# Kernel tuning notes

Hardware: AMD Instinct MI355X
Metric: run time of the kernel (lower is better)

## Reference

```python
import jax, jax.numpy as jnp
import numpy as np

B, S, D, H = 2, 2048, 1024, 16
DH = D // H  # per-head depth = 64


def setup_inputs() -> dict:
    key = jax.random.key(0)
    ks = jax.random.split(key, 10)
    s = 1.0 / np.sqrt(D)
    return {
        "q_in": jax.random.normal(ks[0], (B, S, D), jnp.float32),
        "k_in": jax.random.normal(ks[1], (B, S, D), jnp.float32),
        "v_in": jax.random.normal(ks[2], (B, S, D), jnp.float32),
        "mask": jnp.zeros((B, 1, S, S), jnp.float32),
        "Wq": jax.random.normal(ks[3], (D, D), jnp.float32) * s,
        "bq": jnp.zeros((D,), jnp.float32),
        "Wk": jax.random.normal(ks[4], (D, D), jnp.float32) * s,
        "bk": jnp.zeros((D,), jnp.float32),
        "Wv": jax.random.normal(ks[5], (D, D), jnp.float32) * s,
        "bv": jnp.zeros((D,), jnp.float32),
        "Wo": jax.random.normal(ks[6], (D, D), jnp.float32) * s,
        "bo": jnp.zeros((D,), jnp.float32),
    }


def _split_heads(x):
    # [B,S,D] -> [B,H,S,DH]
    b, s, _ = x.shape
    return x.reshape(b, s, H, DH).transpose(0, 2, 1, 3)


def reference(q_in, k_in, v_in, mask, Wq, bq, Wk, bk, Wv, bv, Wo, bo):
    q = _split_heads(q_in @ Wq + bq)
    k = _split_heads(k_in @ Wk + bk)
    v = _split_heads(v_in @ Wv + bv)
    logits = jnp.einsum("bhqd,bhkd->bhqk", q, k) / jnp.sqrt(jnp.float32(DH))
    logits = logits + mask * -1e9
    attn = jax.nn.softmax(logits, axis=-1)
    ctx = jnp.einsum("bhqk,bhkd->bhqd", attn, v)  # [B,H,S,DH]
    concat = ctx.transpose(0, 2, 1, 3).reshape(q_in.shape[0], -1, D)
    out = concat @ Wo + bo  # dropout is identity at inference
    return out, attn
```

## Files before the change

kernel.cpp:

```cpp
#include <hip/hip_runtime.h>
#include <hip/hip_bf16.h>

static constexpr int cB = 2, cS = 2048, cD = 1024, cH = 16, cDH = 64;

typedef __attribute__((ext_vector_type(4))) float f32x4;
typedef __attribute__((ext_vector_type(8))) short s16x8;
typedef unsigned long long u64;
typedef unsigned short u16;

__device__ inline f32x4 mfma16(s16x8 a, s16x8 b, f32x4 c) {
  return __builtin_amdgcn_mfma_f32_16x16x32_bf16(a, b, c, 0, 0, 0);
}

__device__ inline u16 f2bf(float x) {
  unsigned u = __float_as_uint(x);
  u += 0x7FFFu + ((u >> 16) & 1u);
  return (u16)(u >> 16);
}

__device__ inline unsigned cvt_pk_bf16(float lo, float hi) {
  unsigned r;
  asm("v_cvt_pk_bf16_f32 %0, %1, %2" : "=v"(r) : "v"(lo), "v"(hi));
  return r;
}

__device__ inline f32x4 zero4() { f32x4 z; z[0] = z[1] = z[2] = z[3] = 0.f; return z; }

__device__ inline void gload16(const void* src, void* dst) {
  __builtin_amdgcn_global_load_lds((const __attribute__((address_space(1))) void*)src,
                                   (__attribute__((address_space(3))) void*)dst, 16, 0, 0);
}

__global__ __launch_bounds__(256) void wt4_kernel(const float* __restrict__ W0,
                                                  const float* __restrict__ W1,
                                                  const float* __restrict__ W2,
                                                  const float* __restrict__ W3,
                                                  u16* __restrict__ T0, u16* __restrict__ T1,
                                                  u16* __restrict__ T2, u16* __restrict__ T3) {
  __shared__ float tile[32][33];
  int z = blockIdx.z;
  const float* W = z == 0 ? W0 : z == 1 ? W1 : z == 2 ? W2 : W3;
  u16* Wt = z == 0 ? T0 : z == 1 ? T1 : z == 2 ? T2 : T3;
  int tx = threadIdx.x, ty = threadIdx.y;
  int r0 = blockIdx.y * 32, c0 = blockIdx.x * 32;
  for (int i = ty; i < 32; i += 8)
    tile[i][tx] = W[(size_t)(r0 + i) * cD + c0 + tx];
  __syncthreads();
  for (int i = ty; i < 32; i += 8)
    Wt[(size_t)(c0 + i) * cD + r0 + tx] = f2bf(tile[tx][i]);
}

__global__ __launch_bounds__(256) void maskflag_kernel(const float* __restrict__ mask,
                                                       unsigned char* __restrict__ flags) {
  int blk = blockIdx.x;
  int b = blk >> 10, qt = (blk >> 5) & 31, kt = blk & 31;
  int t = threadIdx.x;
  int r = t >> 2, c0 = (t & 3) * 16;
  const float4* p = (const float4*)(mask + ((size_t)b * cS + qt * 64 + r) * cS + kt * 64 + c0);
  int any = 0;
  for (int j = 0; j < 4; ++j) {
    float4 v = p[j];
    any |= (v.x != 0.f) | (v.y != 0.f) | (v.z != 0.f) | (v.w != 0.f);
  }
  __shared__ int sred;
  if (t == 0) sred = 0;
  __syncthreads();
  if (any) atomicOr(&sred, 1);
  __syncthreads();
  if (t == 0) flags[blk] = (unsigned char)sred;
}

template<bool AFP32, bool OUTF32, int BN>
__device__ __forceinline__ void gemm_body(const void* __restrict__ Ap,
                                          const u16* __restrict__ Bt,
                                          const float* __restrict__ bias,
                                          void* __restrict__ outp,
                                          float scale, int vt_mode, int bidx,
                                          u16* As, u16* Bs) {
  constexpr int NI = BN / 32;
  constexpr int RPW = BN / 4;
  int t = threadIdx.x;
  int w = t >> 6, l = t & 63, g = l >> 4, li = l & 15;
  int bm = bidx & 31, bn = bidx >> 5;
  int m0 = bm * 128, n0 = bn * BN;
  int wr = w >> 1, wc = w & 1;

  f32x4 acc[4][NI];
  for (int i = 0; i < 4; ++i)
    for (int j = 0; j < NI; ++j) acc[i][j] = zero4();

  for (int kk = 0; kk < cD; kk += 64) {
    if (AFP32) {
      const float* X = (const float*)Ap;
      int ar = t >> 1, ak0 = (t & 1) * 32;
      const float* asrc = X + (size_t)(m0 + ar) * cD + kk + ak0;
      int sw = ar & 7;
      for (int j = 0; j < 4; ++j) {
        float4 x0 = ((const float4*)asrc)[2 * j];
        float4 x1 = ((const float4*)asrc)[2 * j + 1];
        union { s16x8 v; unsigned u[4]; } s;
        s.u[0] = cvt_pk_bf16(x0.x, x0.y);
        s.u[1] = cvt_pk_bf16(x0.z, x0.w);
        s.u[2] = cvt_pk_bf16(x1.x, x1.y);
        s.u[3] = cvt_pk_bf16(x1.z, x1.w);
        int chunk = (ak0 >> 3) + j;
        *(s16x8*)&As[ar * 64 + ((chunk ^ sw) * 8)] = s.v;
      }
    } else {
      const u16* X = (const u16*)Ap;
      for (int is = 0; is < 4; ++is) {
        int row = w * 32 + is * 8 + (l >> 3);
        int chunk = l & 7;
        const u16* src = X + (size_t)(m0 + row) * cD + kk + ((chunk ^ (row & 7)) * 8);
        gload16(src, &As[(w * 32 + is * 8) * 64]);
      }
    }
    for (int is = 0; is < RPW / 8; ++is) {
      int row = w * RPW + is * 8 + (l >> 3);
      int chunk = l & 7;
      const u16* src = Bt + (size_t)(n0 + row) * cD + kk + ((chunk ^ (row & 7)) * 8);
      gload16(src, &Bs[(w * RPW + is * 8) * 64]);
    }
    __syncthreads();
    for (int c = 0; c < 2; ++c) {
      s16x8 af[4], bf[NI];
      for (int mi = 0; mi < 4; ++mi) {
        int r = wr * 64 + mi * 16 + li;
        af[mi] = *(const s16x8*)&As[r * 64 + (((c * 4 + g) ^ (r & 7)) * 8)];
      }
      for (int ni = 0; ni < NI; ++ni) {
        int r = wc * (BN / 2) + ni * 16 + li;
        bf[ni] = *(const s16x8*)&Bs[r * 64 + (((c * 4 + g) ^ (r & 7)) * 8)];
      }
      for (int mi = 0; mi < 4; ++mi)
        for (int ni = 0; ni < NI; ++ni)
          acc[mi][ni] = mfma16(af[mi], bf[ni], acc[mi][ni]);
    }
    __syncthreads();
  }

  for (int ni = 0; ni < NI; ++ni) {
    int n = n0 + wc * (BN / 2) + ni * 16 + li;
    float bv = bias[n];
    for (int mi = 0; mi < 4; ++mi) {
      for (int r = 0; r < 4; ++r) {
        int m = m0 + wr * 64 + mi * 16 + g * 4 + r;
        float val = acc[mi][ni][r] + bv;
        if (OUTF32) {
          ((float*)outp)[(size_t)m * cD + n] = val;
        } else {
          val *= scale;
          int b = m >> 11, s = m & 2047;
          int h = n >> 6, d = n & 63;
          size_t idx = vt_mode ? ((size_t)(b * cH + h) * cDH + d) * cS + s
                               : ((size_t)(b * cH + h) * cS + s) * cDH + d;
          ((u16*)outp)[idx] = f2bf(val);
        }
      }
    }
  }
}

__global__ __launch_bounds__(256) void qkv_gemm(const float* __restrict__ Xq,
                                                const float* __restrict__ Xk,
                                                const float* __restrict__ Xv,
                                                const u16* __restrict__ Btq,
                                                const u16* __restrict__ Btk,
                                                const u16* __restrict__ Btv,
                                                const float* __restrict__ bq,
                                                const float* __restrict__ bk,
                                                const float* __restrict__ bv,
                                                u16* __restrict__ oq,
                                                u16* __restrict__ ok,
                                                u16* __restrict__ ov) {
  __shared__ __attribute__((aligned(16))) u16 As[128 * 64];
  __shared__ __attribute__((aligned(16))) u16 Bs[128 * 64];
  int which = blockIdx.x >> 8, bidx = blockIdx.x & 255;
  const float* X = which == 0 ? Xq : which == 1 ? Xk : Xv;
  const u16* Bt = which == 0 ? Btq : which == 1 ? Btk : Btv;
  const float* bias = which == 0 ? bq : which == 1 ? bk : bv;
  u16* o = which == 0 ? oq : which == 1 ? ok : ov;
  float scale = which == 0 ? 0.125f : 1.0f;
  int vt = which == 2 ? 1 : 0;
  gemm_body<true, false, 128>(X, Bt, bias, o, scale, vt, bidx, As, Bs);
}

__global__ __launch_bounds__(256) void out_gemm(const u16* __restrict__ Xc,
                                                const u16* __restrict__ Bt,
                                                const float* __restrict__ bias,
                                                float* __restrict__ outp) {
  __shared__ __attribute__((aligned(16))) u16 As[128 * 64];
  __shared__ __attribute__((aligned(16))) u16 Bs[64 * 64];
  gemm_body<false, true, 64>(Xc, Bt, bias, outp, 1.0f, 0, blockIdx.x, As, Bs);
}

__global__ __launch_bounds__(512) void attn_kernel(const u16* __restrict__ Q,
                                                   const u16* __restrict__ K,
                                                   const u16* __restrict__ Vt,
                                                   const float* __restrict__ mask,
                                                   const unsigned char* __restrict__ flags,
                                                   float* __restrict__ attn,
                                                   u16* __restrict__ ctx) {
  __shared__ __attribute__((aligned(16))) u16 Kl[2][64 * 64];
  __shared__ __attribute__((aligned(16))) u16 Vl[2][64 * 64];
  int t = threadIdx.x;
  int w = t >> 6, l = t & 63, g = l >> 4, li = l & 15;
  int p = blockIdx.x;
  int blk = (p & 7) * 64 + (p >> 3);
  int bh = blk >> 4, qt = blk & 15;
  int b = bh >> 4;
  int qbase = qt * 128;
  const u16* Qh = Q + (size_t)bh * cS * cDH;
  const u16* Kh = K + (size_t)bh * cS * cDH;
  const u16* Vh = Vt + (size_t)bh * cDH * cS;
  const unsigned char* fl = flags + (b << 10) + ((qbase + w * 16) >> 6) * 32;

  s16x8 qf[2];
  {
    const u16* qp = Qh + (size_t)(qbase + w * 16 + li) * cDH;
    qf[0] = *(const s16x8*)(qp + 8 * g);
    qf[1] = *(const s16x8*)(qp + 32 + 8 * g);
  }
  int srow8 = l >> 3, schunk = l & 7;
  int q_lane = qbase + w * 16 + li;
  int srow = w * 8 + srow8;
  const u16* kstage = Kh + (size_t)srow * cDH + ((schunk ^ (srow & 7)) * 8);
  const u16* vstage = Vh + (size_t)srow * cS + ((schunk ^ (srow & 7)) * 8);
  u16* kl_dst = &Kl[0][(w * 8) * 64];
  u16* vl_dst = &Vl[0][(w * 8) * 64];
  const int KSTEP = 64 * cDH;

  gload16(kstage, kl_dst);
  asm volatile("s_waitcnt vmcnt(0)" ::: "memory");
  __builtin_amdgcn_sched_barrier(0);
  __builtin_amdgcn_s_barrier();
  __builtin_amdgcn_sched_barrier(0);
  float racc4[4] = {0.f, 0.f, 0.f, 0.f};
  for (int kt = 0; kt < 32; ++kt) {
    int cur = kt & 1;
    if (kt + 1 < 32)
      gload16(kstage + (size_t)(kt + 1) * KSTEP, kl_dst + (cur ^ 1) * 64 * 64);
    f32x4 acc[4];
    for (int mt = 0; mt < 4; ++mt) acc[mt] = zero4();
    for (int c = 0; c < 2; ++c)
      for (int mt = 0; mt < 4; ++mt) {
        int r = mt * 16 + li;
        s16x8 kf = *(const s16x8*)&Kl[cur][r * 64 + (((c * 4 + g) ^ (r & 7)) * 8)];
        acc[mt] = mfma16(kf, qf[c], acc[mt]);
      }
    bool um = fl[kt] != 0;
    for (int mt = 0; mt < 4; ++mt)
      for (int r = 0; r < 4; ++r) {
        float lv = acc[mt][r];
        if (um) lv += mask[((size_t)b * cS + q_lane) * cS + kt * 64 + mt * 16 + 4 * g + r] * -1e9f;
        racc4[r] += __expf(lv);
      }
    if (kt + 1 < 32) {
      asm volatile("s_waitcnt vmcnt(0)" ::: "memory");
      __builtin_amdgcn_sched_barrier(0);
      __builtin_amdgcn_s_barrier();
      __builtin_amdgcn_sched_barrier(0);
    }
  }
  float racc = (racc4[0] + racc4[1]) + (racc4[2] + racc4[3]);
  racc += __shfl_xor(racc, 16, 64);
  racc += __shfl_xor(racc, 32, 64);
  float lr = __logf(racc);

  f32x4 cacc[4];
  for (int dt = 0; dt < 4; ++dt) cacc[dt] = zero4();
  float* attn_row = attn + (size_t)bh * cS * cS + (size_t)q_lane * cS;
  gload16(kstage, kl_dst);
  gload16(vstage, vl_dst);
  asm volatile("s_waitcnt vmcnt(0)" ::: "memory");
  __builtin_amdgcn_sched_barrier(0);
  __builtin_amdgcn_s_barrier();
  __builtin_amdgcn_sched_barrier(0);
  for (int kt = 0; kt < 32; ++kt) {
    int cur = kt & 1;
    if (kt + 1 < 32) {
      gload16(kstage + (size_t)(kt + 1) * KSTEP, kl_dst + (cur ^ 1) * 64 * 64);
      gload16(vstage + (kt + 1) * 64, vl_dst + (cur ^ 1) * 64 * 64);
    }
    f32x4 acc[4];
    for (int mt = 0; mt < 4; ++mt) acc[mt] = zero4();
    for (int c = 0; c < 2; ++c)
      for (int mt = 0; mt < 4; ++mt) {
        int r = mt * 16 + li;
        s16x8 kf = *(const s16x8*)&Kl[cur][r * 64 + (((c * 4 + g) ^ (r & 7)) * 8)];
        acc[mt] = mfma16(kf, qf[c], acc[mt]);
      }
    bool um = fl[kt] != 0;
    s16x8 pa[2];
    for (int c = 0; c < 2; ++c) {
      union { s16x8 v; unsigned u[4]; } pk;
      f32x4 pvq[2];
      for (int hh = 0; hh < 2; ++hh) {
        int mt = c * 2 + hh;
        for (int r = 0; r < 4; ++r) {
          float lv = acc[mt][r];
          if (um) lv += mask[((size_t)b * cS + q_lane) * cS + kt * 64 + mt * 16 + 4 * g + r] * -1e9f;
          pvq[hh][r] = __expf(lv - lr);
        }
        __builtin_nontemporal_store(pvq[hh], (f32x4*)(attn_row + kt * 64 + mt * 16 + 4 * g));
      }
      pk.u[0] = cvt_pk_bf16(pvq[0][0], pvq[0][1]);
      pk.u[1] = cvt_pk_bf16(pvq[0][2], pvq[0][3]);
      pk.u[2] = cvt_pk_bf16(pvq[1][0], pvq[1][1]);
      pk.u[3] = cvt_pk_bf16(pvq[1][2], pvq[1][3]);
      pa[c] = pk.v;
    }
    for (int c = 0; c < 2; ++c) {
      for (int dt = 0; dt < 4; ++dt) {
        int row = dt * 16 + li;
        const u16* rb = &Vl[cur][row * 64];
        int o0 = (((c * 4 + 0 + (g >> 1)) ^ (li & 7)) * 8) + (g & 1) * 4;
        int o1 = (((c * 4 + 2 + (g >> 1)) ^ (li & 7)) * 8) + (g & 1) * 4;
        union { s16x8 v; u64 qq[2]; } vf;
        vf.qq[0] = *(const u64*)(rb + o0);
        vf.qq[1] = *(const u64*)(rb + o1);
        cacc[dt] = mfma16(pa[c], vf.v, cacc[dt]);
      }
    }
    if (kt + 1 < 32) {
      asm volatile("s_waitcnt vmcnt(4)" ::: "memory");
      __builtin_amdgcn_sched_barrier(0);
      __builtin_amdgcn_s_barrier();
      __builtin_amdgcn_sched_barrier(0);
    }
  }

  int h = bh & 15;
  for (int dt = 0; dt < 4; ++dt)
    for (int r = 0; r < 4; ++r) {
      int s = qbase + w * 16 + g * 4 + r;
      int d = dt * 16 + li;
      ctx[((size_t)(b * cS + s)) * cD + h * 64 + d] = f2bf(cacc[dt][r]);
    }
}

extern "C" void kernel_launch(void* const* d_in, const int* in_sizes, int n_in,
                              void* d_out, int out_size, void* d_ws, size_t ws_size,
                              hipStream_t stream) {
  const float* q_in = (const float*)d_in[0];
  const float* k_in = (const float*)d_in[1];
  const float* v_in = (const float*)d_in[2];
  const float* mask = (const float*)d_in[3];
  const float* Wq = (const float*)d_in[4];
  const float* bq = (const float*)d_in[5];
  const float* Wk = (const float*)d_in[6];
  const float* bk = (const float*)d_in[7];
  const float* Wv = (const float*)d_in[8];
  const float* bv = (const float*)d_in[9];
  const float* Wo = (const float*)d_in[10];
  const float* bo = (const float*)d_in[11];

  float* out = (float*)d_out;
  float* attn = out + (size_t)cB * cS * cD;

  const size_t MATB = (size_t)cB * cS * cD * 2;
  const size_t WB = (size_t)cD * cD * 2;
  char* ws = (char*)d_ws;
  u16* WqT = (u16*)(ws);
  u16* WkT = (u16*)(ws + WB);
  u16* WvT = (u16*)(ws + 2 * WB);
  u16* WoT = (u16*)(ws + 3 * WB);
  u16* wsQ  = (u16*)(ws + 4 * WB);
  u16* wsK  = (u16*)(ws + 4 * WB + MATB);
  u16* wsVt = (u16*)(ws + 4 * WB + 2 * MATB);
  u16* wsC  = (u16*)(ws + 4 * WB + 3 * MATB);
  unsigned char* flags = (unsigned char*)(ws + 4 * WB + 4 * MATB);
  const size_t REQUIRED = 4 * WB + 4 * MATB + 2048;
  if (ws_size < REQUIRED) return;

  dim3 tb(32, 8);
  wt4_kernel<<<dim3(32, 32, 4), tb, 0, stream>>>(Wq, Wk, Wv, Wo, WqT, WkT, WvT, WoT);
  maskflag_kernel<<<2048, 256, 0, stream>>>(mask, flags);

  qkv_gemm<<<768, 256, 0, stream>>>(q_in, k_in, v_in, WqT, WkT, WvT,
                                    bq, bk, bv, wsQ, wsK, wsVt);

  attn_kernel<<<512, 512, 0, stream>>>(wsQ, wsK, wsVt, mask, flags, attn, wsC);

  out_gemm<<<512, 256, 0, stream>>>(wsC, WoT, bo, out);
}
```

Baseline: 336.4 us.

## Pre-convert QKV inputs to bf16 and load via direct global-to-LDS copies

```diff
diff --git a/kernel.cpp b/kernel.cpp
--- a/kernel.cpp
+++ b/kernel.cpp
@@ -29,6 +29,26 @@
 __device__ inline void gload16(const void* src, void* dst) {
   __builtin_amdgcn_global_load_lds((const __attribute__((address_space(1))) void*)src,
                                    (__attribute__((address_space(3))) void*)dst, 16, 0, 0);
+}
+
+__global__ __launch_bounds__(256) void xcvt_kernel(const float* __restrict__ X0,
+                                                   const float* __restrict__ X1,
+                                                   const float* __restrict__ X2,
+                                                   u16* __restrict__ Y0,
+                                                   u16* __restrict__ Y1,
+                                                   u16* __restrict__ Y2) {
+  int z = blockIdx.z;
+  const float* X = z == 0 ? X0 : z == 1 ? X1 : X2;
+  u16* Y = z == 0 ? Y0 : z == 1 ? Y1 : Y2;
+  size_t i = ((size_t)blockIdx.x * 256 + threadIdx.x) * 8;
+  float4 a = *(const float4*)(X + i);
+  float4 b = *(const float4*)(X + i + 4);
+  union { s16x8 v; unsigned u[4]; } s;
+  s.u[0] = cvt_pk_bf16(a.x, a.y);
+  s.u[1] = cvt_pk_bf16(a.z, a.w);
+  s.u[2] = cvt_pk_bf16(b.x, b.y);
+  s.u[3] = cvt_pk_bf16(b.z, b.w);
+  *(s16x8*)(Y + i) = s.v;
 }
 
 __global__ __launch_bounds__(256) void wt4_kernel(const float* __restrict__ W0,
@@ -70,8 +90,8 @@
   if (t == 0) flags[blk] = (unsigned char)sred;
 }
 
-template<bool AFP32, bool OUTF32, int BN>
-__device__ __forceinline__ void gemm_body(const void* __restrict__ Ap,
+template<bool OUTF32, int BN>
+__device__ __forceinline__ void gemm_body(const u16* __restrict__ X,
                                           const u16* __restrict__ Bt,
                                           const float* __restrict__ bias,
                                           void* __restrict__ outp,
@@ -90,30 +110,11 @@
     for (int j = 0; j < NI; ++j) acc[i][j] = zero4();
 
   for (int kk = 0; kk < cD; kk += 64) {
-    if (AFP32) {
-      const float* X = (const float*)Ap;
-      int ar = t >> 1, ak0 = (t & 1) * 32;
-      const float* asrc = X + (size_t)(m0 + ar) * cD + kk + ak0;
-      int sw = ar & 7;
-      for (int j = 0; j < 4; ++j) {
-        float4 x0 = ((const float4*)asrc)[2 * j];
-        float4 x1 = ((const float4*)asrc)[2 * j + 1];
-        union { s16x8 v; unsigned u[4]; } s;
-        s.u[0] = cvt_pk_bf16(x0.x, x0.y);
-        s.u[1] = cvt_pk_bf16(x0.z, x0.w);
-        s.u[2] = cvt_pk_bf16(x1.x, x1.y);
-        s.u[3] = cvt_pk_bf16(x1.z, x1.w);
-        int chunk = (ak0 >> 3) + j;
-        *(s16x8*)&As[ar * 64 + ((chunk ^ sw) * 8)] = s.v;
-      }
-    } else {
-      const u16* X = (const u16*)Ap;
-      for (int is = 0; is < 4; ++is) {
-        int row = w * 32 + is * 8 + (l >> 3);
-        int chunk = l & 7;
-        const u16* src = X + (size_t)(m0 + row) * cD + kk + ((chunk ^ (row & 7)) * 8);
-        gload16(src, &As[(w * 32 + is * 8) * 64]);
-      }
+    for (int is = 0; is < 4; ++is) {
+      int row = w * 32 + is * 8 + (l >> 3);
+      int chunk = l & 7;
+      const u16* src = X + (size_t)(m0 + row) * cD + kk + ((chunk ^ (row & 7)) * 8);
+      gload16(src, &As[(w * 32 + is * 8) * 64]);
     }
     for (int is = 0; is < RPW / 8; ++is) {
       int row = w * RPW + is * 8 + (l >> 3);
@@ -161,9 +162,9 @@
   }
 }
 
-__global__ __launch_bounds__(256) void qkv_gemm(const float* __restrict__ Xq,
-                                                const float* __restrict__ Xk,
-                                                const float* __restrict__ Xv,
+__global__ __launch_bounds__(256) void qkv_gemm(const u16* __restrict__ Xq,
+                                                const u16* __restrict__ Xk,
+                                                const u16* __restrict__ Xv,
                                                 const u16* __restrict__ Btq,
                                                 const u16* __restrict__ Btk,
                                                 const u16* __restrict__ Btv,
@@ -176,13 +177,13 @@
   __shared__ __attribute__((aligned(16))) u16 As[128 * 64];
   __shared__ __attribute__((aligned(16))) u16 Bs[128 * 64];
   int which = blockIdx.x >> 8, bidx = blockIdx.x & 255;
-  const float* X = which == 0 ? Xq : which == 1 ? Xk : Xv;
+  const u16* X = which == 0 ? Xq : which == 1 ? Xk : Xv;
   const u16* Bt = which == 0 ? Btq : which == 1 ? Btk : Btv;
   const float* bias = which == 0 ? bq : which == 1 ? bk : bv;
   u16* o = which == 0 ? oq : which == 1 ? ok : ov;
   float scale = which == 0 ? 0.125f : 1.0f;
   int vt = which == 2 ? 1 : 0;
-  gemm_body<true, false, 128>(X, Bt, bias, o, scale, vt, bidx, As, Bs);
+  gemm_body<false, 128>(X, Bt, bias, o, scale, vt, bidx, As, Bs);
 }
 
 __global__ __launch_bounds__(256) void out_gemm(const u16* __restrict__ Xc,
@@ -191,7 +192,7 @@
                                                 float* __restrict__ outp) {
   __shared__ __attribute__((aligned(16))) u16 As[128 * 64];
   __shared__ __attribute__((aligned(16))) u16 Bs[64 * 64];
-  gemm_body<false, true, 64>(Xc, Bt, bias, outp, 1.0f, 0, blockIdx.x, As, Bs);
+  gemm_body<true, 64>(Xc, Bt, bias, outp, 1.0f, 0, blockIdx.x, As, Bs);
 }
 
 __global__ __launch_bounds__(512) void attn_kernel(const u16* __restrict__ Q,
@@ -302,7 +303,7 @@
           if (um) lv += mask[((size_t)b * cS + q_lane) * cS + kt * 64 + mt * 16 + 4 * g + r] * -1e9f;
           pvq[hh][r] = __expf(lv - lr);
         }
-        __builtin_nontemporal_store(pvq[hh], (f32x4*)(attn_row + kt * 64 + mt * 16 + 4 * g));
+        *(f32x4*)(attn_row + kt * 64 + mt * 16 + 4 * g) = pvq[hh];
       }
       pk.u[0] = cvt_pk_bf16(pvq[0][0], pvq[0][1]);
       pk.u[1] = cvt_pk_bf16(pvq[0][2], pvq[0][3]);
@@ -373,11 +374,18 @@
   const size_t REQUIRED = 4 * WB + 4 * MATB + 2048;
   if (ws_size < REQUIRED) return;
 
+  const size_t XE = (size_t)cB * cS * cD;
+  u16* Xq = (u16*)attn;
+  u16* Xk = Xq + XE;
+  u16* Xv = Xk + XE;
+
   dim3 tb(32, 8);
   wt4_kernel<<<dim3(32, 32, 4), tb, 0, stream>>>(Wq, Wk, Wv, Wo, WqT, WkT, WvT, WoT);
   maskflag_kernel<<<2048, 256, 0, stream>>>(mask, flags);
-
-  qkv_gemm<<<768, 256, 0, stream>>>(q_in, k_in, v_in, WqT, WkT, WvT,
+  xcvt_kernel<<<dim3((unsigned)(XE / 8 / 256), 1, 3), 256, 0, stream>>>(
+      q_in, k_in, v_in, Xq, Xk, Xv);
+
+  qkv_gemm<<<768, 256, 0, stream>>>(Xq, Xk, Xv, WqT, WkT, WvT,
                                     bq, bk, bv, wsQ, wsK, wsVt);
 
   attn_kernel<<<512, 512, 0, stream>>>(wsQ, wsK, wsVt, mask, flags, attn, wsC);
```

Result: faster. 326.4 us (-3.0%).
